# Kernel tuning notes

Measured on AMD Instinct MI355X. Metric: run time of the kernel, lower is better.

The kernel has to match this reference:

```python
import jax, jax.numpy as jnp
import numpy as np

B, C, G, N_OBJ = 256, 1019, 7, 16
IMG_SIZE = 448.0

def setup_inputs() -> dict:
    key = jax.random.key(0)
    k1, k2, k3, k4 = jax.random.split(key, 4)
    outputs = jax.random.normal(k1, (B, 5 + C, G, G), dtype=jnp.float32)
    boxes = jax.random.uniform(k2, (B, N_OBJ, 4), dtype=jnp.float32, minval=0.0, maxval=IMG_SIZE)
    labels = jax.random.randint(k3, (B, N_OBJ), 1, C + 1, dtype=jnp.int32)  # 1..C (code uses label-1)
    coords = jax.random.randint(k4, (B, N_OBJ, 2), 0, G, dtype=jnp.int32)   # (x, y) grid cells
    # objectness target matrix: 1.0 at cells containing an object, else 0 (soft CE target)
    bidx = jnp.arange(B)[:, None]
    obj = jnp.zeros((B, G, G), jnp.float32).at[bidx, coords[..., 1], coords[..., 0]].set(1.0)
    obj_matrix = obj.reshape(B, G * G)
    return {"outputs": outputs, "boxes": boxes, "labels": labels, "coords": coords, "obj_matrix": obj_matrix}

def reference(outputs, boxes, labels, coords, obj_matrix):
    Bn = outputs.shape[0]
    # objectness CE with soft targets: mean over batch of -sum(target * log_softmax(pred))
    p_obj = outputs[:, 0].reshape(Bn, -1)                      # [B, 49]
    cel_obj = jnp.mean(-jnp.sum(obj_matrix * jax.nn.log_softmax(p_obj, axis=-1), axis=-1))
    # gather per-object predictions at grid cells (x=coords[...,0], y=coords[...,1])
    bidx = jnp.arange(Bn)[:, None]
    y = coords[..., 1]
    x = coords[..., 0]
    pred_boxes = outputs[:, 1:5][bidx, :, y, x]                # [B, N_OBJ, 4]
    tgt_scaled = jnp.round(boxes / IMG_SIZE * 10.0) / 10.0     # np.round(x/IMG_SIZE, 1)
    bb_loss = jnp.sum((tgt_scaled - pred_boxes) ** 2) / Bn
    # per-object class cross-entropy, summed then divided by batch
    pred_labels = outputs[:, 5:][bidx, :, y, x]                # [B, N_OBJ, C]
    logp = jax.nn.log_softmax(pred_labels, axis=-1)
    ce = -jnp.take_along_axis(logp, (labels - 1)[..., None].astype(jnp.int32), axis=-1)
    cel_class = jnp.sum(ce) / Bn
    return cel_obj + bb_loss + cel_class
```

## Files before the change

kernel.cpp:

```cpp
#include <hip/hip_runtime.h>

#define BATCH 256
#define NCLS  1019
#define GRID  7
#define NOBJ  16
#define PLANE 49
#define NCH   1024

__global__ __launch_bounds__(256) void yolo_loss_kernel(
    const float* __restrict__ outputs,
    const float* __restrict__ boxes,
    const int*   __restrict__ labels,
    const int*   __restrict__ coords,
    const float* __restrict__ obj_matrix,
    float* __restrict__ out)
{
    const int b    = blockIdx.x;
    const int t    = threadIdx.x;
    const int lane = t & 63;
    const int wave = t >> 6;

    __shared__ int   s_pos[NOBJ];
    __shared__ int   s_cl[NOBJ];
    __shared__ float s_se[NOBJ];
    __shared__ float s_tl[NOBJ];
    __shared__ float s_acc;

    const float* ob = outputs + (size_t)b * NCH * PLANE;

    if (t == 0) s_acc = 0.0f;
    if (t < NOBJ) {
        int x = coords[(b * NOBJ + t) * 2 + 0];
        int y = coords[(b * NOBJ + t) * 2 + 1];
        s_pos[t] = y * GRID + x;
        s_cl[t]  = labels[b * NOBJ + t] - 1;
        s_se[t]  = 0.0f;
    }
    __syncthreads();

    int pos[NOBJ];
#pragma unroll
    for (int o = 0; o < NOBJ; ++o) pos[o] = s_pos[o];
    int cls[NOBJ];
#pragma unroll
    for (int o = 0; o < NOBJ; ++o) cls[o] = s_cl[o];

    float se[NOBJ];
#pragma unroll
    for (int o = 0; o < NOBJ; ++o) se[o] = 0.0f;

    for (int c = t; c < NCLS; c += 256) {
        const float* plane = ob + (size_t)(5 + c) * PLANE;
#pragma unroll
        for (int o = 0; o < NOBJ; ++o) {
            float v = plane[pos[o]];
            se[o] += __expf(v);
            if (c == cls[o]) s_tl[o] = v;
        }
    }
#pragma unroll
    for (int o = 0; o < NOBJ; ++o) {
        float v = se[o];
#pragma unroll
        for (int off = 32; off > 0; off >>= 1)
            v += __shfl_xor(v, off, 64);
        if (lane == 0) atomicAdd(&s_se[o], v);
    }

    if (wave == 0) {
        float l = (lane < PLANE) ? ob[lane] : 0.0f;
        float e = (lane < PLANE) ? __expf(l) : 0.0f;
        float s = e;
#pragma unroll
        for (int off = 32; off > 0; off >>= 1)
            s += __shfl_xor(s, off, 64);
        float lse = __logf(s);
        float m = (lane < PLANE) ? obj_matrix[b * PLANE + lane] : 0.0f;
        float contrib = (lane < PLANE) ? -m * (l - lse) : 0.0f;
#pragma unroll
        for (int off = 32; off > 0; off >>= 1)
            contrib += __shfl_xor(contrib, off, 64);
        if (lane == 0) atomicAdd(&s_acc, contrib);
    }

    if (wave == 1) {
        int o = lane >> 2, k = lane & 3;
        float pred = ob[(size_t)(1 + k) * PLANE + s_pos[o]];
        float tb   = boxes[(b * NOBJ + o) * 4 + k];
        float tgt  = rintf(tb / 448.0f * 10.0f) * 0.1f;
        float d    = tgt - pred;
        float sq   = d * d;
#pragma unroll
        for (int off = 32; off > 0; off >>= 1)
            sq += __shfl_xor(sq, off, 64);
        if (lane == 0) atomicAdd(&s_acc, sq);
    }

    __syncthreads();

    if (t < NOBJ) {
        float ce = __logf(s_se[t]) - s_tl[t];
        atomicAdd(&s_acc, ce);
    }
    __syncthreads();

    if (t == 0) {
        atomicAdd(out, s_acc * (1.0f / (float)BATCH));
    }
}

extern "C" void kernel_launch(void* const* d_in, const int* in_sizes, int n_in,
                              void* d_out, int out_size, void* d_ws, size_t ws_size,
                              hipStream_t stream) {
    const float* outputs    = (const float*)d_in[0];
    const float* boxes      = (const float*)d_in[1];
    const int*   labels     = (const int*)d_in[2];
    const int*   coords     = (const int*)d_in[3];
    const float* obj_matrix = (const float*)d_in[4];
    float* out = (float*)d_out;

    hipMemsetAsync(out, 0, sizeof(float), stream);
    yolo_loss_kernel<<<BATCH, 256, 0, stream>>>(outputs, boxes, labels, coords,
                                                obj_matrix, out);
}
```

Measured before the change: 97.57 us.

## Stream full batch slab with float4 loads and accumulate per-cell exp sums in LDS

Replaces the per-object scattered gathers across class planes with a coalesced float4 sweep of the entire batch slab. Exp values are accumulated per grid cell into shared memory with atomics, and per-object logsumexp is read from the cell it sits in. Block size rises to 1024 threads. This trades extra exp work and LDS atomic contention for coalesced, bandwidth-friendly global reads.

```diff
diff --git a/kernel.cpp b/kernel.cpp
--- a/kernel.cpp
+++ b/kernel.cpp
@@ -6,8 +6,11 @@
 #define NOBJ  16
 #define PLANE 49
 #define NCH   1024
+#define SLAB  (NCH * PLANE)
+#define NVEC  (SLAB / 4)
+#define TPB   1024
 
-__global__ __launch_bounds__(256) void yolo_loss_kernel(
+__global__ __launch_bounds__(TPB) void yolo_loss_kernel(
     const float* __restrict__ outputs,
     const float* __restrict__ boxes,
     const int*   __restrict__ labels,
@@ -20,57 +23,41 @@
     const int lane = t & 63;
     const int wave = t >> 6;
 
+    __shared__ float s_acc[PLANE];
     __shared__ int   s_pos[NOBJ];
     __shared__ int   s_cl[NOBJ];
-    __shared__ float s_se[NOBJ];
-    __shared__ float s_tl[NOBJ];
-    __shared__ float s_acc;
+    __shared__ float s_red;
 
-    const float* ob = outputs + (size_t)b * NCH * PLANE;
-
-    if (t == 0) s_acc = 0.0f;
+    if (t < PLANE) s_acc[t] = 0.0f;
+    if (t == 0)    s_red = 0.0f;
     if (t < NOBJ) {
         int x = coords[(b * NOBJ + t) * 2 + 0];
         int y = coords[(b * NOBJ + t) * 2 + 1];
         s_pos[t] = y * GRID + x;
         s_cl[t]  = labels[b * NOBJ + t] - 1;
-        s_se[t]  = 0.0f;
     }
     __syncthreads();
 
-    int pos[NOBJ];
+    const float*  ob  = outputs + (size_t)b * SLAB;
+    const float4* ob4 = (const float4*)ob;
+
+    for (int vi = t; vi < NVEC; vi += TPB) {
+        float4 v = ob4[vi];
+        int idx = vi * 4;
+        float vals[4] = {v.x, v.y, v.z, v.w};
 #pragma unroll
-    for (int o = 0; o < NOBJ; ++o) pos[o] = s_pos[o];
-    int cls[NOBJ];
-#pragma unroll
-    for (int o = 0; o < NOBJ; ++o) cls[o] = s_cl[o];
-
-    float se[NOBJ];
-#pragma unroll
-    for (int o = 0; o < NOBJ; ++o) se[o] = 0.0f;
-
-    for (int c = t; c < NCLS; c += 256) {
-        const float* plane = ob + (size_t)(5 + c) * PLANE;
-#pragma unroll
-        for (int o = 0; o < NOBJ; ++o) {
-            float v = plane[pos[o]];
-            se[o] += __expf(v);
-            if (c == cls[o]) s_tl[o] = v;
+        for (int j = 0; j < 4; ++j) {
+            int id = idx + j;
+            int c  = id / PLANE;
+            int p  = id - c * PLANE;
+            if (c >= 5) atomicAdd(&s_acc[p], __expf(vals[j]));
         }
     }
-#pragma unroll
-    for (int o = 0; o < NOBJ; ++o) {
-        float v = se[o];
-#pragma unroll
-        for (int off = 32; off > 0; off >>= 1)
-            v += __shfl_xor(v, off, 64);
-        if (lane == 0) atomicAdd(&s_se[o], v);
-    }
+    __syncthreads();
 
     if (wave == 0) {
         float l = (lane < PLANE) ? ob[lane] : 0.0f;
-        float e = (lane < PLANE) ? __expf(l) : 0.0f;
-        float s = e;
+        float s = (lane < PLANE) ? __expf(l) : 0.0f;
 #pragma unroll
         for (int off = 32; off > 0; off >>= 1)
             s += __shfl_xor(s, off, 64);
@@ -80,33 +67,32 @@
 #pragma unroll
         for (int off = 32; off > 0; off >>= 1)
             contrib += __shfl_xor(contrib, off, 64);
-        if (lane == 0) atomicAdd(&s_acc, contrib);
+        if (lane == 0) atomicAdd(&s_red, contrib);
     }
 
     if (wave == 1) {
         int o = lane >> 2, k = lane & 3;
         float pred = ob[(size_t)(1 + k) * PLANE + s_pos[o]];
         float tb   = boxes[(b * NOBJ + o) * 4 + k];
-        float tgt  = rintf(tb / 448.0f * 10.0f) * 0.1f;
+        float tgt  = rintf(tb * (10.0f / 448.0f)) * 0.1f;
         float d    = tgt - pred;
         float sq   = d * d;
 #pragma unroll
         for (int off = 32; off > 0; off >>= 1)
             sq += __shfl_xor(sq, off, 64);
-        if (lane == 0) atomicAdd(&s_acc, sq);
+        if (lane == 0) atomicAdd(&s_red, sq);
+    }
+
+    if (wave == 2 && lane < NOBJ) {
+        int   o  = lane;
+        float se = s_acc[s_pos[o]];
+        float tl = ob[(size_t)(5 + s_cl[o]) * PLANE + s_pos[o]];
+        float ce = __logf(se) - tl;
+        atomicAdd(&s_red, ce);
     }
 
     __syncthreads();
-
-    if (t < NOBJ) {
-        float ce = __logf(s_se[t]) - s_tl[t];
-        atomicAdd(&s_acc, ce);
-    }
-    __syncthreads();
-
-    if (t == 0) {
-        atomicAdd(out, s_acc * (1.0f / (float)BATCH));
-    }
+    if (t == 0) atomicAdd(out, s_red * (1.0f / (float)BATCH));
 }
 
 extern "C" void kernel_launch(void* const* d_in, const int* in_sizes, int n_in,
@@ -120,6 +106,6 @@
     float* out = (float*)d_out;
 
     hipMemsetAsync(out, 0, sizeof(float), stream);
-    yolo_loss_kernel<<<BATCH, 256, 0, stream>>>(outputs, boxes, labels, coords,
+    yolo_loss_kernel<<<BATCH, TPB, 0, stream>>>(outputs, boxes, labels, coords,
                                                 obj_matrix, out);
 }
```

Result: slower. 148.2 us (+51.9%).
